# Performance work log

Hardware: AMD Instinct MI355X
Metric: run time of the kernel (lower is better)

## Reference

```python
import jax, jax.numpy as jnp
import numpy as np

N_LAYERS = 2
NUM_BRANCHES = 3
TOPK_START = 10
TOPK_END = 3


def normalize_adj(adj):
    # symmetric degree normalization: D^-1/2 (A + I) D^-1/2
    n = adj.shape[0]
    a = jnp.clip(adj + jnp.eye(n, dtype=adj.dtype), 1e-8, jnp.inf)
    row_sum = jnp.clip(a.sum(axis=1), 1e-8, jnp.inf)
    d = jnp.clip(row_sum ** -0.5, 0.0, 100.0)
    return d[:, None] * a * d[None, :]


def setup_inputs() -> dict:
    key = jax.random.key(0)
    k1, k2 = jax.random.split(key)
    B, T, N, C = 512, 16, 22, 64
    x = jax.random.normal(k1, (B, T, N, C), dtype=jnp.float32)
    # emulate nn.Parameter init: clamp(adj,0,1)*0.01 + 0.05*I
    raw = jax.random.uniform(k2, (N, N), dtype=jnp.float32)
    adj = jnp.clip(raw, 0.0, 1.0) * 0.01 + 0.05 * jnp.eye(N, dtype=jnp.float32)
    branch_temps = jnp.ones((NUM_BRANCHES,), dtype=jnp.float32)
    fusion_logits = jnp.zeros((N_LAYERS, NUM_BRANCHES), dtype=jnp.float32)
    return {"x": x, "adj": adj, "branch_temps": branch_temps, "fusion_logits": fusion_logits}


def reference(x, adj, branch_temps, fusion_logits):
    B, T, N, C = x.shape
    # [B, T, N, C] -> [B, N, T*C]
    x0 = jnp.transpose(x, (0, 2, 1, 3)).reshape(B, N, T * C)
    A = normalize_adj(jnp.clip(adj, 0.0, 1.0))          # [N, N]
    temps = jnp.clip(branch_temps, 0.1, 10.0)           # [nb]
    eye = jnp.eye(N, dtype=x0.dtype)

    xb = x0
    for layer in range(N_LAYERS):
        K = int(TOPK_START - (TOPK_START - TOPK_END) * (layer / max(1, N_LAYERS - 1)))
        K = min(K, N)
        alpha = jax.nn.softmax(fusion_logits[layer])    # [nb]
        # cosine similarity, masked by normalized adjacency
        xn = xb / (jnp.linalg.norm(xb, axis=-1, keepdims=True) + 1e-6)
        sim = jnp.einsum('bnd,bmd->bnm', xn, xn) * A    # [B, N, N]
        # per-branch temperature + diagonal boost
        att = sim[None] / temps[:, None, None, None] + 0.1 * eye  # [nb, B, N, N]
        # annealed top-k sparsification (zeros still participate in softmax, as in torch)
        _, idx = jax.lax.top_k(att, K)                  # [nb, B, N, K]
        mask = jax.nn.one_hot(idx, N, dtype=att.dtype).sum(axis=-2)  # [nb, B, N, N]
        att = jax.nn.softmax(att * mask, axis=-1)
        y = jnp.einsum('kbnm,bmd->kbnd', att, xb)       # branch aggregation
        xb = jnp.einsum('k,kbnd->bnd', alpha, y)        # fusion
        if layer > 0:
            xb = xb + x0
        if layer < N_LAYERS - 1:
            xb = jax.nn.relu(xb)  # dropout identity in eval mode
    return xb, A
```

## Files before the change

### kernel.cpp

```cpp
#include <hip/hip_runtime.h>
#include <hip/hip_bf16.h>

#define BATCH  512
#define TT     16
#define NN     22
#define CC     64
#define DD     1024
#define NB     3
#define XS     1032
#define NTHR   512
#define WPAD   40

typedef __bf16 bf16x8 __attribute__((ext_vector_type(8)));
typedef float  f32x4  __attribute__((ext_vector_type(4)));
typedef float  f32x16 __attribute__((ext_vector_type(16)));
typedef short  s16x8  __attribute__((ext_vector_type(8)));

__device__ __forceinline__ unsigned bf16rne(float x) {
  unsigned u = __float_as_uint(x);
  u += 0x7fffu + ((u >> 16) & 1u);
  return u >> 16;
}
__device__ __forceinline__ unsigned pack2(float a, float b) {
  return bf16rne(a) | (bf16rne(b) << 16);
}

__global__ __launch_bounds__(NTHR) void mbdsca_fused(
    const float* __restrict__ x,
    const float* __restrict__ adj,
    const float* __restrict__ btemps,
    const float* __restrict__ flogits,
    float* __restrict__ out)
{
  __shared__ unsigned short xs[NN][XS];
  __shared__ float As[NN][NN];
  __shared__ float Gp[4][NN][NN];
  __shared__ float attB[NB][NN][NN];
  __shared__ float mxs[NB][NN];
  __shared__ float sinv[NB][NN];
  __shared__ unsigned short Wh[32][WPAD];
  __shared__ unsigned short Wl[32][WPAD];
  __shared__ float dnorm[NN];
  __shared__ float alphas[2][NB];
  __shared__ float tvals[NB];

  const int tid  = threadIdx.x;
  const int b    = blockIdx.x;
  const int lane = tid & 63;
  const int wv   = tid >> 6;

  if (tid < NN * NN) {
    int n = tid / NN, m = tid - n * NN;
    float v = adj[tid];
    v = fminf(fmaxf(v, 0.0f), 1.0f);
    if (n == m) v += 1.0f;
    As[n][m] = fmaxf(v, 1e-8f);
  }
  if (tid < NB) tvals[tid] = fminf(fmaxf(btemps[tid], 0.1f), 10.0f);
  for (int i = tid; i < 32 * WPAD / 2; i += NTHR) {
    ((unsigned*)Wh)[i] = 0u;
    ((unsigned*)Wl)[i] = 0u;
  }
  __syncthreads();

  if (tid < NN) {
    float s = 0.0f;
    for (int m = 0; m < NN; ++m) s += As[tid][m];
    s = fmaxf(s, 1e-8f);
    dnorm[tid] = fminf(fmaxf(1.0f / sqrtf(s), 0.0f), 100.0f);
  }
  if (tid == 0) {
    for (int l = 0; l < 2; ++l) {
      float l0 = flogits[l*NB+0], l1 = flogits[l*NB+1], l2 = flogits[l*NB+2];
      float mx = fmaxf(l0, fmaxf(l1, l2));
      float e0 = __expf(l0-mx), e1 = __expf(l1-mx), e2 = __expf(l2-mx);
      float s = e0 + e1 + e2;
      alphas[l][0] = e0/s; alphas[l][1] = e1/s; alphas[l][2] = e2/s;
    }
  }
  __syncthreads();

  if (tid < NN * NN) {
    int n = tid / NN, m = tid - n * NN;
    As[n][m] = dnorm[n] * As[n][m] * dnorm[m];
  }
  #pragma unroll
  for (int j = 0; j < 11; ++j) {
    int f4  = tid + j * NTHR;
    int t   = f4 / (NN * (CC/4));
    int rem = f4 - t * (NN * (CC/4));
    int n   = rem >> 4;
    int c4  = rem & 15;
    const float4 v = *(const float4*)(&x[(size_t)b * (TT*NN*CC) + (size_t)f4 * 4]);
    uint2 p; p.x = pack2(v.x, v.y); p.y = pack2(v.z, v.w);
    *(uint2*)(&xs[n][t * CC + c4 * 4]) = p;
  }
  __syncthreads();

  for (int layer = 0; layer < 2; ++layer) {
    const int K = (layer == 0) ? 10 : 3;

    if (wv < 4) {
      int row = lane & 31; if (row > NN-1) row = NN-1;
      const int hi = lane >> 5;
      f32x16 acc0 = {}, acc1 = {};
      #pragma unroll
      for (int s = 0; s < 16; ++s) {
        int ks = wv * 16 + s;
        bf16x8 a = *(const bf16x8*)(&xs[row][ks * 16 + hi * 8]);
        if (s & 1) acc1 = __builtin_amdgcn_mfma_f32_32x32x16_bf16(a, a, acc1, 0, 0, 0);
        else       acc0 = __builtin_amdgcn_mfma_f32_32x32x16_bf16(a, a, acc0, 0, 0, 0);
      }
      #pragma unroll
      for (int r = 0; r < 16; ++r) {
        float v = acc0[r] + acc1[r];
        int orow = (r & 3) + 8 * (r >> 2) + 4 * hi;
        int ocol = lane & 31;
        if (orow < NN && ocol < NN) Gp[wv][orow][ocol] = v;
      }
    }
    __syncthreads();

    if (tid < NN) {
      float gn = Gp[0][tid][tid] + Gp[1][tid][tid] + Gp[2][tid][tid] + Gp[3][tid][tid];
      dnorm[tid] = 1.0f / (sqrtf(gn) + 1e-6f);
    }
    __syncthreads();

    if (tid < NN * NN) {
      int n = tid / NN, m = tid - n * NN;
      float g = Gp[0][n][m] + Gp[1][n][m] + Gp[2][n][m] + Gp[3][n][m];
      Gp[0][n][m] = g * dnorm[n] * dnorm[m] * As[n][m];
    }
    __syncthreads();

    for (int q = tid; q < NB * NN * NN; q += NTHR) {
      int k = q / (NN*NN), r = q - k * (NN*NN);
      int n = r / NN, m = r - n * NN;
      const float rtk = 1.0f / tvals[k];
      float v = Gp[0][n][m] * rtk + ((n == m) ? 0.1f : 0.0f);
      int rank = 0; float rmax = -1e30f;
      #pragma unroll
      for (int j = 0; j < NN; ++j) {
        float vj = Gp[0][n][j] * rtk + ((n == j) ? 0.1f : 0.0f);
        rank += (vj > v) || (vj == v && j < m);
        rmax = fmaxf(rmax, vj);
      }
      attB[k][n][m] = (rank < K) ? v : 0.0f;
      if (m == 0) mxs[k][n] = fmaxf(rmax, 0.0f);
    }
    __syncthreads();

    if (tid < NB * NN) {
      int k = tid / NN, n = tid - k * NN;
      float mx = mxs[k][n], s = 0.0f;
      for (int m = 0; m < NN; ++m) s += __expf(attB[k][n][m] - mx);
      sinv[k][n] = alphas[layer][k] / s;
    }
    __syncthreads();

    if (tid < NN * NN) {
      int n = tid / NN, m = tid - n * NN;
      float w = 0.0f;
      #pragma unroll
      for (int k = 0; k < NB; ++k)
        w += __expf(attB[k][n][m] - mxs[k][n]) * sinv[k][n];
      unsigned h = bf16rne(w);
      float wh = __uint_as_float(h << 16);
      Wh[n][m] = (unsigned short)h;
      Wl[n][m] = (unsigned short)bf16rne(w - wh);
    }
    __syncthreads();

    {
      const int wr = lane & 15;
      const int kg = lane >> 4;
      bf16x8 ah0 = *(const bf16x8*)(&Wh[wr][kg * 8]);
      bf16x8 al0 = *(const bf16x8*)(&Wl[wr][kg * 8]);
      bf16x8 ah1 = *(const bf16x8*)(&Wh[16 + wr][kg * 8]);
      bf16x8 al1 = *(const bf16x8*)(&Wl[16 + wr][kg * 8]);
      #pragma unroll 2
      for (int i = 0; i < 8; ++i) {
        const int Nt   = wv + i * 8;
        const int dcol = Nt * 16 + wr;
        s16x8 bsv;
        #pragma unroll
        for (int j = 0; j < 8; ++j) {
          int m  = kg * 8 + j;
          int mc = (m < NN) ? m : 0;
          bsv[j] = (short)xs[mc][dcol];
        }
        bf16x8 bfr = __builtin_bit_cast(bf16x8, bsv);
        f32x4 y0 = {}, y1 = {};
        y0 = __builtin_amdgcn_mfma_f32_16x16x32_bf16(al0, bfr, y0, 0, 0, 0);
        y0 = __builtin_amdgcn_mfma_f32_16x16x32_bf16(ah0, bfr, y0, 0, 0, 0);
        y1 = __builtin_amdgcn_mfma_f32_16x16x32_bf16(al1, bfr, y1, 0, 0, 0);
        y1 = __builtin_amdgcn_mfma_f32_16x16x32_bf16(ah1, bfr, y1, 0, 0, 0);
        if (layer == 0) {
          #pragma unroll
          for (int r = 0; r < 4; ++r) {
            int row0 = kg * 4 + r;
            xs[row0][dcol] = (unsigned short)bf16rne(fmaxf(y0[r], 0.0f));
          }
          #pragma unroll
          for (int r = 0; r < 4; ++r) {
            int row1 = 16 + kg * 4 + r;
            if (row1 < NN)
              xs[row1][dcol] = (unsigned short)bf16rne(fmaxf(y1[r], 0.0f));
          }
        } else {
          const float* xres = x + (size_t)b * (TT*NN*CC);
          const int t = dcol >> 6, c = dcol & 63;
          float* ob = out + (size_t)b * (NN*DD) + dcol;
          #pragma unroll
          for (int r = 0; r < 4; ++r) {
            int row0 = kg * 4 + r;
            ob[row0 * DD] = y0[r] + xres[(t * NN + row0) * CC + c];
          }
          #pragma unroll
          for (int r = 0; r < 4; ++r) {
            int row1 = 16 + kg * 4 + r;
            if (row1 < NN)
              ob[row1 * DD] = y1[r] + xres[(t * NN + row1) * CC + c];
          }
        }
      }
    }
    __syncthreads();
  }

  if (b == 0 && tid < NN * NN) {
    out[(size_t)BATCH * NN * DD + tid] = As[tid / NN][tid - (tid / NN) * NN];
  }
}

extern "C" void kernel_launch(void* const* d_in, const int* in_sizes, int n_in,
                              void* d_out, int out_size, void* d_ws, size_t ws_size,
                              hipStream_t stream) {
  const float* x       = (const float*)d_in[0];
  const float* adj     = (const float*)d_in[1];
  const float* btemps  = (const float*)d_in[2];
  const float* flogits = (const float*)d_in[3];
  float* out = (float*)d_out;
  mbdsca_fused<<<BATCH, NTHR, 0, stream>>>(x, adj, btemps, flogits, out);
}
```

Measured before the change: 63.21 us.

## Retile shared activations for transposed LDS reads and vectorized aggregation MFMA

Stores the bf16 activations in a blocked 16-column tile layout so the aggregation step can fetch B-operands with ds_read_b64_tr_b16 instead of scalar gathers. That step now uses 32x32x16 MFMAs, so each lane writes four contiguous values and can issue vector float4 residual loads and output stores. The norm computation is folded into the similarity pass, and the top-k ranking handles all three branches in one thread per element, which drops a couple of barriers. The risk is added inline-asm complexity and a hard s_waitcnt that serialises the LDS reads.

```diff
diff --git a/kernel.cpp b/kernel.cpp
--- a/kernel.cpp
+++ b/kernel.cpp
@@ -7,14 +7,12 @@
 #define CC     64
 #define DD     1024
 #define NB     3
-#define XS     1032
 #define NTHR   512
 #define WPAD   40
 
 typedef __bf16 bf16x8 __attribute__((ext_vector_type(8)));
 typedef float  f32x4  __attribute__((ext_vector_type(4)));
 typedef float  f32x16 __attribute__((ext_vector_type(16)));
-typedef short  s16x8  __attribute__((ext_vector_type(8)));
 
 __device__ __forceinline__ unsigned bf16rne(float x) {
   unsigned u = __float_as_uint(x);
@@ -23,6 +21,9 @@
 }
 __device__ __forceinline__ unsigned pack2(float a, float b) {
   return bf16rne(a) | (bf16rne(b) << 16);
+}
+__device__ __forceinline__ unsigned xoff(unsigned m, unsigned d) {
+  return ((d >> 4) * 6u + (m >> 2)) * 64u + (m & 3u) * 16u + (d & 15u);
 }
 
 __global__ __launch_bounds__(NTHR) void mbdsca_fused(
@@ -32,15 +33,16 @@
     const float* __restrict__ flogits,
     float* __restrict__ out)
 {
-  __shared__ unsigned short xs[NN][XS];
+  __shared__ unsigned short xs[6 * 64 * 64];
   __shared__ float As[NN][NN];
   __shared__ float Gp[4][NN][NN];
+  __shared__ float simS[NN][NN];
   __shared__ float attB[NB][NN][NN];
   __shared__ float mxs[NB][NN];
   __shared__ float sinv[NB][NN];
   __shared__ unsigned short Wh[32][WPAD];
   __shared__ unsigned short Wl[32][WPAD];
-  __shared__ float dnorm[NN];
+  __shared__ float deg[NN];
   __shared__ float alphas[2][NB];
   __shared__ float tvals[NB];
 
@@ -67,7 +69,7 @@
     float s = 0.0f;
     for (int m = 0; m < NN; ++m) s += As[tid][m];
     s = fmaxf(s, 1e-8f);
-    dnorm[tid] = fminf(fmaxf(1.0f / sqrtf(s), 0.0f), 100.0f);
+    deg[tid] = fminf(fmaxf(1.0f / sqrtf(s), 0.0f), 100.0f);
   }
   if (tid == 0) {
     for (int l = 0; l < 2; ++l) {
@@ -82,7 +84,7 @@
 
   if (tid < NN * NN) {
     int n = tid / NN, m = tid - n * NN;
-    As[n][m] = dnorm[n] * As[n][m] * dnorm[m];
+    As[n][m] = deg[n] * As[n][m] * deg[m];
   }
   #pragma unroll
   for (int j = 0; j < 11; ++j) {
@@ -93,9 +95,16 @@
     int c4  = rem & 15;
     const float4 v = *(const float4*)(&x[(size_t)b * (TT*NN*CC) + (size_t)f4 * 4]);
     uint2 p; p.x = pack2(v.x, v.y); p.y = pack2(v.z, v.w);
-    *(uint2*)(&xs[n][t * CC + c4 * 4]) = p;
+    *(uint2*)(&xs[xoff(n, t * 64 + c4 * 4)]) = p;
+  }
+  {
+    int m  = 22 + (tid >> 8);
+    int d0 = (tid & 255) * 4;
+    *(uint2*)(&xs[xoff(m, d0)]) = make_uint2(0u, 0u);
   }
   __syncthreads();
+
+  const unsigned xsb = (unsigned)(unsigned long long)(void*)&xs[0];
 
   for (int layer = 0; layer < 2; ++layer) {
     const int K = (layer == 0) ? 10 : 3;
@@ -106,55 +115,67 @@
       f32x16 acc0 = {}, acc1 = {};
       #pragma unroll
       for (int s = 0; s < 16; ++s) {
-        int ks = wv * 16 + s;
-        bf16x8 a = *(const bf16x8*)(&xs[row][ks * 16 + hi * 8]);
+        int d0 = (wv * 16 + s) * 16 + hi * 8;
+        bf16x8 a = *(const bf16x8*)(&xs[xoff(row, d0)]);
         if (s & 1) acc1 = __builtin_amdgcn_mfma_f32_32x32x16_bf16(a, a, acc1, 0, 0, 0);
         else       acc0 = __builtin_amdgcn_mfma_f32_32x32x16_bf16(a, a, acc0, 0, 0, 0);
       }
       #pragma unroll
       for (int r = 0; r < 16; ++r) {
-        float v = acc0[r] + acc1[r];
+        float vv = acc0[r] + acc1[r];
         int orow = (r & 3) + 8 * (r >> 2) + 4 * hi;
         int ocol = lane & 31;
-        if (orow < NN && ocol < NN) Gp[wv][orow][ocol] = v;
-      }
-    }
-    __syncthreads();
-
-    if (tid < NN) {
-      float gn = Gp[0][tid][tid] + Gp[1][tid][tid] + Gp[2][tid][tid] + Gp[3][tid][tid];
-      dnorm[tid] = 1.0f / (sqrtf(gn) + 1e-6f);
+        if (orow < NN && ocol < NN) Gp[wv][orow][ocol] = vv;
+      }
     }
     __syncthreads();
 
     if (tid < NN * NN) {
       int n = tid / NN, m = tid - n * NN;
-      float g = Gp[0][n][m] + Gp[1][n][m] + Gp[2][n][m] + Gp[3][n][m];
-      Gp[0][n][m] = g * dnorm[n] * dnorm[m] * As[n][m];
-    }
-    __syncthreads();
-
-    for (int q = tid; q < NB * NN * NN; q += NTHR) {
-      int k = q / (NN*NN), r = q - k * (NN*NN);
-      int n = r / NN, m = r - n * NN;
-      const float rtk = 1.0f / tvals[k];
-      float v = Gp[0][n][m] * rtk + ((n == m) ? 0.1f : 0.0f);
-      int rank = 0; float rmax = -1e30f;
+      float g  = Gp[0][n][m] + Gp[1][n][m] + Gp[2][n][m] + Gp[3][n][m];
+      float gn = Gp[0][n][n] + Gp[1][n][n] + Gp[2][n][n] + Gp[3][n][n];
+      float gm = Gp[0][m][m] + Gp[1][m][m] + Gp[2][m][m] + Gp[3][m][m];
+      float rn = 1.0f / (sqrtf(gn) + 1e-6f);
+      float rm = 1.0f / (sqrtf(gm) + 1e-6f);
+      simS[n][m] = g * rn * rm * As[n][m];
+    }
+    __syncthreads();
+
+    if (tid < NN * NN) {
+      const int n = tid / NN, m = tid - n * NN;
+      float simrow[NN];
+      float simn = 0.f, simm = 0.f, rmax_ex = -1e30f;
       #pragma unroll
       for (int j = 0; j < NN; ++j) {
-        float vj = Gp[0][n][j] * rtk + ((n == j) ? 0.1f : 0.0f);
-        rank += (vj > v) || (vj == v && j < m);
-        rmax = fmaxf(rmax, vj);
-      }
-      attB[k][n][m] = (rank < K) ? v : 0.0f;
-      if (m == 0) mxs[k][n] = fmaxf(rmax, 0.0f);
+        float s = simS[n][j];
+        simrow[j] = s;
+        simn = (j == n) ? s : simn;
+        simm = (j == m) ? s : simm;
+        rmax_ex = (j == n) ? rmax_ex : fmaxf(rmax_ex, s);
+      }
+      #pragma unroll
+      for (int k = 0; k < NB; ++k) {
+        const float tk  = tvals[k];
+        const float rtk = 1.0f / tk;
+        const float vn  = simn + 0.1f * tk;
+        const float vown = (m == n) ? vn : simm;
+        int rank = 0;
+        #pragma unroll
+        for (int j = 0; j < NN; ++j) {
+          float vj = (j == n) ? vn : simrow[j];
+          rank += (vj > vown) || (vj == vown && j < m);
+        }
+        attB[k][n][m] = (rank < K) ? vown * rtk : 0.0f;
+        if (m == 0) mxs[k][n] = fmaxf(fmaxf(rmax_ex, vn) * rtk, 0.0f);
+      }
     }
     __syncthreads();
 
     if (tid < NB * NN) {
       int k = tid / NN, n = tid - k * NN;
       float mx = mxs[k][n], s = 0.0f;
-      for (int m = 0; m < NN; ++m) s += __expf(attB[k][n][m] - mx);
+      #pragma unroll
+      for (int m2 = 0; m2 < NN; ++m2) s += __expf(attB[k][n][m2] - mx);
       sinv[k][n] = alphas[layer][k] / s;
     }
     __syncthreads();
@@ -166,62 +187,65 @@
       for (int k = 0; k < NB; ++k)
         w += __expf(attB[k][n][m] - mxs[k][n]) * sinv[k][n];
       unsigned h = bf16rne(w);
-      float wh = __uint_as_float(h << 16);
       Wh[n][m] = (unsigned short)h;
-      Wl[n][m] = (unsigned short)bf16rne(w - wh);
+      Wl[n][m] = (unsigned short)bf16rne(w - __uint_as_float(h << 16));
     }
     __syncthreads();
 
     {
-      const int wr = lane & 15;
-      const int kg = lane >> 4;
-      bf16x8 ah0 = *(const bf16x8*)(&Wh[wr][kg * 8]);
-      bf16x8 al0 = *(const bf16x8*)(&Wl[wr][kg * 8]);
-      bf16x8 ah1 = *(const bf16x8*)(&Wh[16 + wr][kg * 8]);
-      bf16x8 al1 = *(const bf16x8*)(&Wl[16 + wr][kg * 8]);
-      #pragma unroll 2
-      for (int i = 0; i < 8; ++i) {
-        const int Nt   = wv + i * 8;
-        const int dcol = Nt * 16 + wr;
-        s16x8 bsv;
-        #pragma unroll
-        for (int j = 0; j < 8; ++j) {
-          int m  = kg * 8 + j;
-          int mc = (m < NN) ? m : 0;
-          bsv[j] = (short)xs[mc][dcol];
-        }
-        bf16x8 bfr = __builtin_bit_cast(bf16x8, bsv);
-        f32x4 y0 = {}, y1 = {};
-        y0 = __builtin_amdgcn_mfma_f32_16x16x32_bf16(al0, bfr, y0, 0, 0, 0);
-        y0 = __builtin_amdgcn_mfma_f32_16x16x32_bf16(ah0, bfr, y0, 0, 0, 0);
-        y1 = __builtin_amdgcn_mfma_f32_16x16x32_bf16(al1, bfr, y1, 0, 0, 0);
-        y1 = __builtin_amdgcn_mfma_f32_16x16x32_bf16(ah1, bfr, y1, 0, 0, 0);
-        if (layer == 0) {
-          #pragma unroll
-          for (int r = 0; r < 4; ++r) {
-            int row0 = kg * 4 + r;
-            xs[row0][dcol] = (unsigned short)bf16rne(fmaxf(y0[r], 0.0f));
-          }
-          #pragma unroll
-          for (int r = 0; r < 4; ++r) {
-            int row1 = 16 + kg * 4 + r;
-            if (row1 < NN)
-              xs[row1][dcol] = (unsigned short)bf16rne(fmaxf(y1[r], 0.0f));
-          }
-        } else {
-          const float* xres = x + (size_t)b * (TT*NN*CC);
-          const int t = dcol >> 6, c = dcol & 63;
-          float* ob = out + (size_t)b * (NN*DD) + dcol;
-          #pragma unroll
-          for (int r = 0; r < 4; ++r) {
-            int row0 = kg * 4 + r;
-            ob[row0 * DD] = y0[r] + xres[(t * NN + row0) * CC + c];
-          }
-          #pragma unroll
-          for (int r = 0; r < 4; ++r) {
-            int row1 = 16 + kg * 4 + r;
-            if (row1 < NN)
-              ob[row1 * DD] = y1[r] + xres[(t * NN + row1) * CC + c];
+      const int n_b = lane & 31;
+      const int ko  = (lane >> 5) * 8;
+      bf16x8 w0h = *(const bf16x8*)(&Wh[n_b][ko]);
+      bf16x8 w0l = *(const bf16x8*)(&Wl[n_b][ko]);
+      bf16x8 w1h = *(const bf16x8*)(&Wh[n_b][16 + ko]);
+      bf16x8 w1l = *(const bf16x8*)(&Wl[n_b][16 + ko]);
+      const int dpr     = lane & 31;
+      const int dsub_in = dpr >> 4;
+      const int dcol    = dpr & 15;
+      const int hi5     = lane >> 5;
+      unsigned mqA  = (unsigned)(hi5 * 2);
+      unsigned mqB0 = 4 + mqA;  if (mqB0 > 5) mqB0 = 5;
+      unsigned mqB1 = 5 + mqA;  if (mqB1 > 5) mqB1 = 5;
+      #pragma unroll
+      for (int i = 0; i < 4; ++i) {
+        const int dtile = wv * 4 + i;
+        const unsigned rowb = xsb + (unsigned)(dtile * 2 + dsub_in) * 6u * 128u + (unsigned)dcol * 8u;
+        unsigned long long t00, t01, t10, t11;
+        asm volatile("ds_read_b64_tr_b16 %0, %1" : "=v"(t00) : "v"(rowb + mqA * 128u));
+        asm volatile("ds_read_b64_tr_b16 %0, %1" : "=v"(t01) : "v"(rowb + (mqA + 1u) * 128u));
+        asm volatile("ds_read_b64_tr_b16 %0, %1" : "=v"(t10) : "v"(rowb + mqB0 * 128u));
+        asm volatile("ds_read_b64_tr_b16 %0, %1" : "=v"(t11) : "v"(rowb + mqB1 * 128u));
+        asm volatile("s_waitcnt lgkmcnt(0)" ::: "memory");
+        __builtin_amdgcn_sched_barrier(0);
+        int4 a0i = make_int4((int)t00, (int)(t00 >> 32), (int)t01, (int)(t01 >> 32));
+        int4 a1i = make_int4((int)t10, (int)(t10 >> 32), (int)t11, (int)(t11 >> 32));
+        bf16x8 A0 = __builtin_bit_cast(bf16x8, a0i);
+        bf16x8 A1 = __builtin_bit_cast(bf16x8, a1i);
+        f32x16 acc = {};
+        acc = __builtin_amdgcn_mfma_f32_32x32x16_bf16(A0, w0h, acc, 0, 0, 0);
+        acc = __builtin_amdgcn_mfma_f32_32x32x16_bf16(A0, w0l, acc, 0, 0, 0);
+        acc = __builtin_amdgcn_mfma_f32_32x32x16_bf16(A1, w1h, acc, 0, 0, 0);
+        acc = __builtin_amdgcn_mfma_f32_32x32x16_bf16(A1, w1l, acc, 0, 0, 0);
+        if (n_b < NN) {
+          if (layer == 0) {
+            #pragma unroll
+            for (int q = 0; q < 4; ++q) {
+              int dq = dtile * 32 + 4 * hi5 + 8 * q;
+              uint2 p;
+              p.x = pack2(fmaxf(acc[4*q+0], 0.f), fmaxf(acc[4*q+1], 0.f));
+              p.y = pack2(fmaxf(acc[4*q+2], 0.f), fmaxf(acc[4*q+3], 0.f));
+              *(uint2*)(&xs[xoff(n_b, dq)]) = p;
+            }
+          } else {
+            #pragma unroll
+            for (int q = 0; q < 4; ++q) {
+              int dq = dtile * 32 + 4 * hi5 + 8 * q;
+              int t = dq >> 6, c = dq & 63;
+              const float4 r = *(const float4*)(&x[(size_t)b * (TT*NN*CC) + (t * NN + n_b) * CC + c]);
+              float4 o = make_float4(acc[4*q+0] + r.x, acc[4*q+1] + r.y,
+                                     acc[4*q+2] + r.z, acc[4*q+3] + r.w);
+              *(float4*)(&out[((size_t)b * NN + n_b) * DD + dq]) = o;
+            }
           }
         }
       }
```

Result: faster. 51.66 us (median of 2 runs) (-18.3%).
